# Kernel tuning notes

Hardware: AMD Instinct MI355X
Metric: run time of the kernel (lower is better)

## Reference

```python
import jax, jax.numpy as jnp
import numpy as np

N = 2048
H_DIM = 64
N_HEADS = 4
N_HIDDEN = H_DIM // N_HEADS  # is_concat=True
L = 16  # max_labels_dim
SLOPE = 0.2


def leaky(x, slope=SLOPE):
    return jnp.where(x >= 0, x, slope * x)


def setup_inputs() -> dict:
    key = jax.random.key(0)
    k1, k2, k3, k4 = jax.random.split(key, 4)
    x = jax.random.normal(k1, (N, H_DIM), dtype=jnp.float32)
    # labels in [0, L]; value == L means unlabeled -> all-zero one-hot row
    lab = jax.random.randint(k2, (N,), 0, L + 1)
    ohm_labels = jnp.where((lab < L)[:, None],
                           jax.nn.one_hot(jnp.minimum(lab, L - 1), L, dtype=jnp.float32),
                           0.0)
    in_features = H_DIM + L
    W_l = jax.random.normal(k3, (H_DIM, in_features), dtype=jnp.float32) / np.sqrt(in_features)
    W_attn = jax.random.normal(k4, (N_HIDDEN,), dtype=jnp.float32) / np.sqrt(N_HIDDEN)
    return {"x": x, "ohm_labels": ohm_labels, "W_l": W_l, "W_attn": W_attn, "sparsity": 0}


def reference(x, ohm_labels, W_l, W_attn, sparsity):
    n_nodes = x.shape[0]
    # fill unlabeled rows with uniform 1/L
    unlabeled = ohm_labels.sum(axis=1) == 0  # (N,)
    ohm = jnp.where(unlabeled[:, None], 1.0 / L, ohm_labels)
    pin = jnp.concatenate([x, ohm], axis=1)  # (N, h_dim + L)

    # shared-weight projection: g_l == g_r == g
    g = (pin @ W_l.T).reshape(n_nodes, N_HEADS, N_HIDDEN)  # (N, H, F)
    # g_sum[i, j] = g_l[j] + g_r[i]  (repeat / repeat_interleave semantics)
    g_sum = g[None, :, :, :] + g[:, None, :, :]            # (N, N, H, F)
    e = jnp.einsum('ijhf,f->ijh', leaky(g_sum), W_attn)    # (N, N, H)
    a = jax.nn.softmax(e, axis=1)                          # softmax over j
    # dropout in eval mode: identity
    attn_res = jnp.einsum('ijh,jhf->ihf', a, g)            # (N, H, F)
    out = attn_res.reshape(n_nodes, N_HEADS * N_HIDDEN)    # is_concat
    h = leaky(out)                                         # processor activation

    # centroids per label from ohm (post-fill) as in get_centroids
    cluster_agg = ohm.T @ h                                # (L, D)
    cnt = ohm.sum(axis=0)                                  # (L,)
    missing = cnt == 0
    centroids = jnp.where(missing[:, None], 0.0,
                          cluster_agg / jnp.where(missing, 1.0, cnt)[:, None])
    # cdist p=2
    diff = h[:, None, :] - centroids[None, :, :]           # (N, L, D)
    scores = -jnp.sqrt(jnp.sum(diff * diff, axis=-1))      # (N, L)
    return scores, h, missing
```

## Files before the change

### kernel.cpp

```cpp
#include <hip/hip_runtime.h>
#include <hip/hip_bf16.h>
#include <math.h>

#define C1F  0.577078016f
#define C2F  0.865617024f

#define WS_CNT 0
#define WS_AGG 128
#define WS_G   8320
#define WS_DCL (8320 + 524288)

typedef float __attribute__((ext_vector_type(4))) f32x4;

__device__ __forceinline__ float rfl(float x) {
    return __uint_as_float(__builtin_amdgcn_readfirstlane(__float_as_uint(x)));
}

__device__ __forceinline__ float dpp_sum(float x) {
    float y;
    y = __int_as_float(__builtin_amdgcn_update_dpp(0, __float_as_int(x), 0x111, 0xf, 0xf, true)); x += y;
    y = __int_as_float(__builtin_amdgcn_update_dpp(0, __float_as_int(x), 0x112, 0xf, 0xf, true)); x += y;
    y = __int_as_float(__builtin_amdgcn_update_dpp(0, __float_as_int(x), 0x114, 0xf, 0xf, true)); x += y;
    y = __int_as_float(__builtin_amdgcn_update_dpp(0, __float_as_int(x), 0x118, 0xf, 0xf, true)); x += y;
    y = __int_as_float(__builtin_amdgcn_update_dpp(0, __float_as_int(x), 0x142, 0xa, 0xf, true)); x += y;
    y = __int_as_float(__builtin_amdgcn_update_dpp(0, __float_as_int(x), 0x143, 0xc, 0xf, true)); x += y;
    return x;
}

__global__ __launch_bounds__(256) void k_proj(
    const float* __restrict__ x, const float* __restrict__ ohm,
    const float* __restrict__ Wl, const float* __restrict__ Wattn,
    unsigned char* __restrict__ ws)
{
    float* g2   = (float*)(ws + WS_G);
    float* dclT = (float*)(ws + WS_DCL);
    unsigned long long* cnt = (unsigned long long*)(ws + WS_CNT);

    int t = threadIdx.x;
    int r = blockIdx.x * 4 + (t >> 6);
    int o = t & 63;

    f32x4 oh[4]; float rs = 0.f;
    const f32x4* ohp = (const f32x4*)&ohm[r*16];
    #pragma unroll
    for (int q = 0; q < 4; ++q) { oh[q] = ohp[q]; rs += oh[q][0]+oh[q][1]+oh[q][2]+oh[q][3]; }
    if (rs == 0.f) {
        f32x4 c = {0.0625f, 0.0625f, 0.0625f, 0.0625f};
        #pragma unroll
        for (int q = 0; q < 4; ++q) oh[q] = c;
    }

    float acc = 0.f;
    const f32x4* xp = (const f32x4*)&x[r*64];
    const f32x4* wp = (const f32x4*)&Wl[o*80];
    #pragma unroll
    for (int q = 0; q < 16; ++q) {
        f32x4 a = xp[q], b = wp[q];
        acc = fmaf(a[0],b[0],acc); acc = fmaf(a[1],b[1],acc);
        acc = fmaf(a[2],b[2],acc); acc = fmaf(a[3],b[3],acc);
    }
    #pragma unroll
    for (int q = 0; q < 4; ++q) {
        f32x4 b = wp[16+q];
        acc = fmaf(oh[q][0],b[0],acc); acc = fmaf(oh[q][1],b[1],acc);
        acc = fmaf(oh[q][2],b[2],acc); acc = fmaf(oh[q][3],b[3],acc);
    }
    g2[(o >> 4)*32768 + (o & 15)*2048 + r] = acc;

    float dot = Wattn[o & 15] * acc;
    #pragma unroll
    for (int m2 = 1; m2 < 16; m2 <<= 1) dot += __shfl_xor(dot, m2);
    if ((o & 15) == 0) dclT[(o >> 4)*2048 + r] = C2F * dot;

    if (t < 16) {
        float c = 0.f;
        for (int rr = 0; rr < 4; ++rr) {
            int r2 = blockIdx.x*4 + rr; float s = 0.f;
            #pragma unroll
            for (int k = 0; k < 16; ++k) s += ohm[r2*16+k];
            c += (s == 0.f) ? 0.0625f : ohm[r2*16+t];
        }
        atomicAdd(&cnt[t], (unsigned long long)__float2ll_rn(c * 1048576.0f));
    }
}

__global__ __launch_bounds__(256, 2) void k_attn(
    const float* __restrict__ ohm, const float* __restrict__ Wattn,
    unsigned char* __restrict__ ws, float* __restrict__ hout)
{
    float* g2   = (float*)(ws + WS_G);
    float* dclT = (float*)(ws + WS_DCL);
    unsigned long long* agg = (unsigned long long*)(ws + WS_AGG);

    __shared__ float shh[128];
    __shared__ float ohmf[32];

    int t = threadIdx.x, bid = blockIdx.x;
    int h = t >> 6, l = t & 63;
    int i0 = bid*2, i1 = i0 + 1;

    const float* g2h = g2 + h*32768;
    const float* dpt = dclT + h*2048;

    float wv[16], gA0[16], gA1[16];
    #pragma unroll
    for (int f = 0; f < 16; ++f) {
        wv[f]  = rfl(Wattn[f]);
        gA0[f] = rfl(g2h[f*2048 + i0]);
        gA1[f] = rfl(g2h[f*2048 + i1]);
    }

    float acc0[16], acc1[16];
    float l0 = 0.f, l1 = 0.f;
    #pragma unroll
    for (int f = 0; f < 16; ++f) { acc0[f] = 0.f; acc1[f] = 0.f; }

    for (int pass = 0; pass < 8; ++pass) {
        int jb = pass*256 + 4*l;
        f32x4 G[16];
        #pragma unroll
        for (int f = 0; f < 16; ++f) G[f] = *(const f32x4*)&g2h[f*2048 + jb];
        f32x4 dj = *(const f32x4*)&dpt[jb];

        float e00=0.f,e01=0.f,e02=0.f,e03=0.f;
        float e10=0.f,e11=0.f,e12=0.f,e13=0.f;
        #pragma unroll
        for (int f = 0; f < 16; ++f) {
            float a0 = gA0[f], a1 = gA1[f];
            f32x4 gf = G[f];
            e00 = fmaf(wv[f], fabsf(a0 + gf[0]), e00);
            e01 = fmaf(wv[f], fabsf(a0 + gf[1]), e01);
            e02 = fmaf(wv[f], fabsf(a0 + gf[2]), e02);
            e03 = fmaf(wv[f], fabsf(a0 + gf[3]), e03);
            e10 = fmaf(wv[f], fabsf(a1 + gf[0]), e10);
            e11 = fmaf(wv[f], fabsf(a1 + gf[1]), e11);
            e12 = fmaf(wv[f], fabsf(a1 + gf[2]), e12);
            e13 = fmaf(wv[f], fabsf(a1 + gf[3]), e13);
        }
        float p00 = __builtin_amdgcn_exp2f(fmaf(C1F, e00, dj[0]));
        float p01 = __builtin_amdgcn_exp2f(fmaf(C1F, e01, dj[1]));
        float p02 = __builtin_amdgcn_exp2f(fmaf(C1F, e02, dj[2]));
        float p03 = __builtin_amdgcn_exp2f(fmaf(C1F, e03, dj[3]));
        float p10 = __builtin_amdgcn_exp2f(fmaf(C1F, e10, dj[0]));
        float p11 = __builtin_amdgcn_exp2f(fmaf(C1F, e11, dj[1]));
        float p12 = __builtin_amdgcn_exp2f(fmaf(C1F, e12, dj[2]));
        float p13 = __builtin_amdgcn_exp2f(fmaf(C1F, e13, dj[3]));
        l0 += (p00 + p01) + (p02 + p03);
        l1 += (p10 + p11) + (p12 + p13);
        #pragma unroll
        for (int f = 0; f < 16; ++f) {
            f32x4 gf = G[f];
            acc0[f] = fmaf(p00, gf[0], fmaf(p01, gf[1],
                      fmaf(p02, gf[2], fmaf(p03, gf[3], acc0[f]))));
            acc1[f] = fmaf(p10, gf[0], fmaf(p11, gf[1],
                      fmaf(p12, gf[2], fmaf(p13, gf[3], acc1[f]))));
        }
    }

    float ls0 = dpp_sum(l0), ls1 = dpp_sum(l1);
    float h0[16], h1[16];
    #pragma unroll
    for (int f = 0; f < 16; ++f) { h0[f] = dpp_sum(acc0[f]); h1[f] = dpp_sum(acc1[f]); }

    if (l == 63) {
        float r0 = 1.0f / ls0, r1 = 1.0f / ls1;
        #pragma unroll
        for (int f = 0; f < 16; ++f) {
            float a = h0[f]*r0; a = fmaxf(a, 0.2f*a);
            float b = h1[f]*r1; b = fmaxf(b, 0.2f*b);
            hout[i0*64 + h*16 + f] = a;
            hout[i1*64 + h*16 + f] = b;
            shh[       h*16 + f] = a;
            shh[64 +   h*16 + f] = b;
        }
    }
    if (t < 32) {
        int rr = t >> 4, ll = t & 15;
        float v = ohm[(bid*2 + rr)*16 + ll];
        float s = v;
        #pragma unroll
        for (int m2 = 1; m2 < 16; m2 <<= 1) s += __shfl_xor(s, m2);
        ohmf[rr*16 + ll] = (s == 0.f) ? 0.0625f : v;
    }
    __syncthreads();

    for (int v = t; v < 1024; v += 256) {
        int ll = v >> 6, d = v & 63;
        float s = fmaf(ohmf[ll], shh[d], ohmf[16 + ll] * shh[64 + d]);
        atomicAdd(&agg[v], (unsigned long long)__float2ll_rn(s * 67108864.0f));
    }
}

__global__ __launch_bounds__(256) void k_scores(
    unsigned char* __restrict__ ws, const float* __restrict__ hout,
    float* __restrict__ scores, float* __restrict__ missing)
{
    __shared__ float cl[16*68];
    unsigned long long* cnt = (unsigned long long*)(ws + WS_CNT);
    unsigned long long* agg = (unsigned long long*)(ws + WS_AGG);
    int t = threadIdx.x;

    for (int v = t; v < 1024; v += 256) {
        int ll = v >> 6, d = v & 63;
        long long a = (long long)agg[v];
        long long c = (long long)cnt[ll];
        cl[ll*68 + d] = (c == 0) ? 0.f : ((float)a / (float)c) * 0.015625f;
    }
    if (blockIdx.x == 0 && t < 16) missing[t] = (cnt[t] == 0) ? 1.0f : 0.0f;
    __syncthreads();

    int i = blockIdx.x*16 + (t >> 4), ll = t & 15;
    float s = 0.f;
    #pragma unroll 16
    for (int d = 0; d < 64; ++d) {
        float diff = hout[i*64 + d] - cl[ll*68 + d];
        s = fmaf(diff, diff, s);
    }
    scores[i*16 + ll] = -sqrtf(s);
}

extern "C" void kernel_launch(void* const* d_in, const int* in_sizes, int n_in,
                              void* d_out, int out_size, void* d_ws, size_t ws_size,
                              hipStream_t stream)
{
    const float* x     = (const float*)d_in[0];
    const float* ohm   = (const float*)d_in[1];
    const float* Wl    = (const float*)d_in[2];
    const float* Wattn = (const float*)d_in[3];
    unsigned char* ws  = (unsigned char*)d_ws;

    float* out     = (float*)d_out;
    float* scores  = out;
    float* hout    = out + 2048*16;
    float* missing = out + 2048*16 + 2048*64;

    hipMemsetAsync(d_ws, 0, 8320, stream);
    k_proj  <<<512,  256, 0, stream>>>(x, ohm, Wl, Wattn, ws);
    k_attn  <<<1024, 256, 0, stream>>>(ohm, Wattn, ws, hout);
    k_scores<<<128,  256, 0, stream>>>(ws, hout, scores, missing);
}
```

Before: 64.65 us.

## Stage per-head projection into LDS and reduce centroid atomics per 32-row block

The attention kernel now runs 1024-thread blocks. Each block handles one head and 32 query rows, and first copies that head's whole g slice and the dcl vector into shared memory, so the inner loop reads LDS instead of global or L2. Each block then reduces its 32 rows' label-weighted contributions in shared memory before issuing one atomic per (label, feature) pair, which cuts global 64-bit atomics sharply. The cost is about 140KB of LDS per block, so only one block fits per CU. The 1024-thread launch bound also caps VGPRs per thread, which may cause spills or reduce latency hiding.

```diff
diff --git a/kernel.cpp b/kernel.cpp
--- a/kernel.cpp
+++ b/kernel.cpp
@@ -84,7 +84,7 @@
     }
 }
 
-__global__ __launch_bounds__(256, 2) void k_attn(
+__global__ __launch_bounds__(1024, 1) void k_attn(
     const float* __restrict__ ohm, const float* __restrict__ Wattn,
     unsigned char* __restrict__ ws, float* __restrict__ hout)
 {
@@ -92,16 +92,27 @@
     float* dclT = (float*)(ws + WS_DCL);
     unsigned long long* agg = (unsigned long long*)(ws + WS_AGG);
 
-    __shared__ float shh[128];
-    __shared__ float ohmf[32];
+    __shared__ float g2l[16*2048];
+    __shared__ float djl[2048];
+    __shared__ float shh[32*16];
+    __shared__ float ohmf[32*16];
 
     int t = threadIdx.x, bid = blockIdx.x;
-    int h = t >> 6, l = t & 63;
-    int i0 = bid*2, i1 = i0 + 1;
+    int h  = bid >> 6;
+    int ib = (bid & 63) * 32;
+    int wid = t >> 6, l = t & 63;
+    int i0 = ib + wid*2, i1 = i0 + 1;
 
     const float* g2h = g2 + h*32768;
-    const float* dpt = dclT + h*2048;
-
+    const float* dph = dclT + h*2048;
+
+    {
+        const f32x4* s4 = (const f32x4*)g2h;
+        f32x4* d4 = (f32x4*)g2l;
+        #pragma unroll
+        for (int c = 0; c < 8; ++c) d4[t + c*1024] = s4[t + c*1024];
+        if (t < 512) ((f32x4*)djl)[t] = ((const f32x4*)dph)[t];
+    }
     float wv[16], gA0[16], gA1[16];
     #pragma unroll
     for (int f = 0; f < 16; ++f) {
@@ -109,6 +120,7 @@
         gA0[f] = rfl(g2h[f*2048 + i0]);
         gA1[f] = rfl(g2h[f*2048 + i1]);
     }
+    __syncthreads();
 
     float acc0[16], acc1[16];
     float l0 = 0.f, l1 = 0.f;
@@ -119,8 +131,8 @@
         int jb = pass*256 + 4*l;
         f32x4 G[16];
         #pragma unroll
-        for (int f = 0; f < 16; ++f) G[f] = *(const f32x4*)&g2h[f*2048 + jb];
-        f32x4 dj = *(const f32x4*)&dpt[jb];
+        for (int f = 0; f < 16; ++f) G[f] = *(const f32x4*)&g2l[f*2048 + jb];
+        f32x4 dj = *(const f32x4*)&djl[jb];
 
         float e00=0.f,e01=0.f,e02=0.f,e03=0.f;
         float e10=0.f,e11=0.f,e12=0.f,e13=0.f;
@@ -170,24 +182,28 @@
             float b = h1[f]*r1; b = fmaxf(b, 0.2f*b);
             hout[i0*64 + h*16 + f] = a;
             hout[i1*64 + h*16 + f] = b;
-            shh[       h*16 + f] = a;
-            shh[64 +   h*16 + f] = b;
-        }
-    }
-    if (t < 32) {
-        int rr = t >> 4, ll = t & 15;
-        float v = ohm[(bid*2 + rr)*16 + ll];
+            shh[(wid*2    )*16 + f] = a;
+            shh[(wid*2 + 1)*16 + f] = b;
+        }
+    }
+    if (t < 512) {
+        int r = t >> 4, lab = t & 15;
+        float v = ohm[(ib + r)*16 + lab];
         float s = v;
         #pragma unroll
         for (int m2 = 1; m2 < 16; m2 <<= 1) s += __shfl_xor(s, m2);
-        ohmf[rr*16 + ll] = (s == 0.f) ? 0.0625f : v;
+        ohmf[r*16 + lab] = (s == 0.f) ? 0.0625f : v;
     }
     __syncthreads();
 
-    for (int v = t; v < 1024; v += 256) {
-        int ll = v >> 6, d = v & 63;
-        float s = fmaf(ohmf[ll], shh[d], ohmf[16 + ll] * shh[64 + d]);
-        atomicAdd(&agg[v], (unsigned long long)__float2ll_rn(s * 67108864.0f));
+    if (t < 256) {
+        int lab = t >> 4, dq = t & 15;
+        float s = 0.f;
+        #pragma unroll 8
+        for (int r = 0; r < 32; ++r)
+            s = fmaf(ohmf[r*16 + lab], shh[r*16 + dq], s);
+        atomicAdd(&agg[lab*64 + h*16 + dq],
+                  (unsigned long long)__float2ll_rn(s * 67108864.0f));
     }
 }
 
@@ -235,7 +251,7 @@
     float* missing = out + 2048*16 + 2048*64;
 
     hipMemsetAsync(d_ws, 0, 8320, stream);
-    k_proj  <<<512,  256, 0, stream>>>(x, ohm, Wl, Wattn, ws);
-    k_attn  <<<1024, 256, 0, stream>>>(ohm, Wattn, ws, hout);
-    k_scores<<<128,  256, 0, stream>>>(ws, hout, scores, missing);
-}
+    k_proj  <<<512, 256, 0, stream>>>(x, ohm, Wl, Wattn, ws);
+    k_attn  <<<256, 1024, 0, stream>>>(ohm, Wattn, ws, hout);
+    k_scores<<<128, 256, 0, stream>>>(ws, hout, scores, missing);
+}
```

Result: faster. 55.22 us (-14.6%).
